# Optimization experiments

Measured on AMD Instinct MI355X. Metric: run time of the kernel, lower is better.

The kernel has to match this reference:

```python
import jax, jax.numpy as jnp
import numpy as np

V, D, H, L, S, B, FF, MAXLEN = 50257, 768, 12, 12, 1024, 4, 3072, 1024
HD = D // H
EPS = 1e-5


def layernorm(x, w, b):
    m = jnp.mean(x, axis=-1, keepdims=True)
    v = jnp.mean(jnp.square(x - m), axis=-1, keepdims=True)
    return (x - m) * jax.lax.rsqrt(v + EPS) * w + b


def setup_inputs() -> dict:
    key = jax.random.key(0)
    ks = jax.random.split(key, 8)
    std = 0.02
    return {
        "tokens": jax.random.randint(ks[0], (B, S), 0, V, dtype=jnp.int32),
        "wte": std * jax.random.normal(ks[1], (V, D), jnp.float32),
        "wpe": std * jax.random.normal(ks[2], (1, MAXLEN, D), jnp.float32),
        "ln1_w": jnp.ones((L, D), jnp.float32),
        "ln1_b": jnp.zeros((L, D), jnp.float32),
        "ln2_w": jnp.ones((L, D), jnp.float32),
        "ln2_b": jnp.zeros((L, D), jnp.float32),
        "W_exp": std * jax.random.normal(ks[3], (L, D, 3 * D), jnp.float32),
        "b_exp": jnp.zeros((L, 3 * D), jnp.float32),
        "W_o": std * jax.random.normal(ks[4], (L, D, D), jnp.float32),
        "b_o": jnp.zeros((L, D), jnp.float32),
        "W_ff1": std * jax.random.normal(ks[5], (L, D, FF), jnp.float32),
        "b_ff1": jnp.zeros((L, FF), jnp.float32),
        "W_ff2": std * jax.random.normal(ks[6], (L, FF, D), jnp.float32),
        "b_ff2": jnp.zeros((L, D), jnp.float32),
    }


def reference(tokens, wte, wpe, ln1_w, ln1_b, ln2_w, ln2_b,
              W_exp, b_exp, W_o, b_o, W_ff1, b_ff1, W_ff2, b_ff2):
    Bc, Sc = tokens.shape
    x = wte[tokens] + wpe[:, :Sc, :]                      # [B,S,D]
    mask = jnp.tril(jnp.ones((Sc, Sc), bool))             # causal (past=None)
    scale = 1.0 / jnp.sqrt(jnp.float32(HD))
    presents = []
    for l in range(L):
        h = layernorm(x, ln1_w[l], ln1_b[l])
        qkv = h @ W_exp[l] + b_exp[l]                     # [B,S,3D]
        q, k, v = jnp.split(qkv, 3, axis=-1)
        q = q.reshape(Bc, Sc, H, HD)
        k = k.reshape(Bc, Sc, H, HD)
        v = v.reshape(Bc, Sc, H, HD)
        presents.append(jnp.stack([k, v]))                # [2,B,S,H,HD]
        score = jnp.einsum('bqhd,bkhd->bhqk', q, k)
        score = jnp.where(mask, score, jnp.float32(-1e20))
        attn = jax.nn.softmax(score * scale, axis=-1)     # mask applied BEFORE scaling, as in source
        a = jnp.einsum('bhqk,bkhd->bqhd', attn, v).reshape(Bc, Sc, D)
        a = a @ W_o[l] + b_o[l]
        add = layernorm(a + x, ln2_w[l], ln2_b[l])        # LN2 on residual sum (GPT2-variant in source)
        ff = jax.nn.gelu(add @ W_ff1[l] + b_ff1[l], approximate=False)
        ff = ff @ W_ff2[l] + b_ff2[l]
        x = ff + add
    return x, jnp.stack(presents)                         # [L,2,B,S,H,HD]
```

## Files before the change

### kernel.cpp

```cpp
#include <hip/hip_runtime.h>
#include <hip/hip_bf16.h>
#include <math.h>

#define Bc 4
#define Sc 1024
#define Dc 768
#define Hc 12
#define Lc 12
#define FFc 3072
#define Mtot (Bc*Sc)

typedef __bf16 bf16x8 __attribute__((ext_vector_type(8)));
typedef __bf16 bf16x4 __attribute__((ext_vector_type(4)));
typedef float f32x4 __attribute__((ext_vector_type(4)));

__device__ __forceinline__ void gload_lds16(const void* g, void* l) {
    __builtin_amdgcn_global_load_lds((const __attribute__((address_space(1))) void*)g,
                                     (__attribute__((address_space(3))) void*)l, 16, 0, 0);
}

template <int N>
__device__ __forceinline__ void waitcnt_vm() {
    if constexpr (N == 0)       asm volatile("s_waitcnt vmcnt(0)" ::: "memory");
    else if constexpr (N == 4)  asm volatile("s_waitcnt vmcnt(4)" ::: "memory");
    else if constexpr (N == 5)  asm volatile("s_waitcnt vmcnt(5)" ::: "memory");
    else if constexpr (N == 8)  asm volatile("s_waitcnt vmcnt(8)" ::: "memory");
    else if constexpr (N == 10) asm volatile("s_waitcnt vmcnt(10)" ::: "memory");
    else static_assert(N == 0, "unsupported vmcnt");
}

__global__ __launch_bounds__(256) void embed_kernel(const int* __restrict__ tokens,
                                                    const float* __restrict__ wte,
                                                    const float* __restrict__ wpe,
                                                    float* __restrict__ x) {
    int row = blockIdx.x;
    int s = row & (Sc - 1);
    int tok = tokens[row];
    const float* wt = wte + (size_t)tok * Dc;
    const float* wp = wpe + (size_t)s * Dc;
    float* xr = x + (size_t)row * Dc;
#pragma unroll
    for (int k = 0; k < 3; ++k) {
        int d = threadIdx.x + k * 256;
        xr[d] = wt[d] + wp[d];
    }
}

__global__ __launch_bounds__(256) void prep_kernel(
        const float* __restrict__ We, const float* __restrict__ Wo,
        const float* __restrict__ Wf1, const float* __restrict__ Wf2,
        __bf16* __restrict__ Te, __bf16* __restrict__ To,
        __bf16* __restrict__ Tf1, __bf16* __restrict__ Tf2,
        const float* __restrict__ x, const float* __restrict__ lw,
        const float* __restrict__ lb, __bf16* __restrict__ outb) {
    __shared__ float shm[64 * 69];
    int bid = blockIdx.x;
    int t = threadIdx.x;
    if (bid < 1728) {
        const float* W; __bf16* T; int K, N, tt;
        if (bid < 432)       { W = We;  T = Te;  K = 768;  N = 2304; tt = bid; }
        else if (bid < 576)  { W = Wo;  T = To;  K = 768;  N = 768;  tt = bid - 432; }
        else if (bid < 1152) { W = Wf1; T = Tf1; K = 768;  N = 3072; tt = bid - 576; }
        else                 { W = Wf2; T = Tf2; K = 3072; N = 768;  tt = bid - 1152; }
        int nx = N >> 6;
        int n0 = (tt % nx) * 64, k0 = (tt / nx) * 64;
        int cx = (t & 15) * 4, ry = t >> 4;
#pragma unroll
        for (int i = 0; i < 4; ++i) {
            int r = ry + 16 * i;
            float4 v = *(const float4*)(W + (size_t)(k0 + r) * N + n0 + cx);
            shm[r * 69 + cx + 0] = v.x; shm[r * 69 + cx + 1] = v.y;
            shm[r * 69 + cx + 2] = v.z; shm[r * 69 + cx + 3] = v.w;
        }
        __syncthreads();
        int kc = (t & 15) * 4, ny = t >> 4;
#pragma unroll
        for (int i = 0; i < 4; ++i) {
            int nr = ny + 16 * i;
            bf16x4 o;
#pragma unroll
            for (int j = 0; j < 4; ++j)
                o[j] = (__bf16)shm[(kc + j) * 69 + nr];
            *(bf16x4*)(T + (size_t)(n0 + nr) * K + k0 + kc) = o;
        }
    } else {
        int row = bid - 1728;
        size_t ro = (size_t)row * Dc;
        float4 v;
        float s1 = 0.0f, s2 = 0.0f;
        if (t < 192) {
            v = *(const float4*)(x + ro + t * 4);
            s1 = v.x + v.y + v.z + v.w;
            s2 = v.x * v.x + v.y * v.y + v.z * v.z + v.w * v.w;
#pragma unroll
            for (int o = 32; o; o >>= 1) {
                s1 += __shfl_down(s1, o);
                s2 += __shfl_down(s2, o);
            }
            if ((t & 63) == 0) { shm[t >> 6] = s1; shm[3 + (t >> 6)] = s2; }
        }
        __syncthreads();
        if (t < 192) {
            float S1 = shm[0] + shm[1] + shm[2];
            float S2 = shm[3] + shm[4] + shm[5];
            float mean = S1 * (1.0f / Dc);
            float var = S2 * (1.0f / Dc) - mean * mean;
            float rs = rsqrtf(var + 1e-5f);
            const float4 w4 = *(const float4*)(lw + t * 4);
            const float4 b4 = *(const float4*)(lb + t * 4);
            bf16x4 o;
            o[0] = (__bf16)((v.x - mean) * rs * w4.x + b4.x);
            o[1] = (__bf16)((v.y - mean) * rs * w4.y + b4.y);
            o[2] = (__bf16)((v.z - mean) * rs * w4.z + b4.z);
            o[3] = (__bf16)((v.w - mean) * rs * w4.w + b4.w);
            *(bf16x4*)(outb + ro + t * 4) = o;
        }
    }
}

__global__ __launch_bounds__(192) void ln2_kernel(const float* __restrict__ x,
                                                  const float* __restrict__ lw,
                                                  const float* __restrict__ lb,
                                                  __bf16* __restrict__ outb,
                                                  float* __restrict__ outf) {
    __shared__ float red[6];
    int row = blockIdx.x;
    size_t ro = (size_t)row * Dc;
    int t = threadIdx.x;
    float4 v = *(const float4*)(x + ro + t * 4);
    float s1 = v.x + v.y + v.z + v.w;
    float s2 = v.x * v.x + v.y * v.y + v.z * v.z + v.w * v.w;
#pragma unroll
    for (int o = 32; o; o >>= 1) {
        s1 += __shfl_down(s1, o);
        s2 += __shfl_down(s2, o);
    }
    if ((t & 63) == 0) { red[t >> 6] = s1; red[3 + (t >> 6)] = s2; }
    __syncthreads();
    float S1 = red[0] + red[1] + red[2];
    float S2 = red[3] + red[4] + red[5];
    float mean = S1 * (1.0f / Dc);
    float var = S2 * (1.0f / Dc) - mean * mean;
    float rs = rsqrtf(var + 1e-5f);
    const float4 w4 = *(const float4*)(lw + t * 4);
    const float4 b4 = *(const float4*)(lb + t * 4);
    float o0 = (v.x - mean) * rs * w4.x + b4.x;
    float o1 = (v.y - mean) * rs * w4.y + b4.y;
    float o2 = (v.z - mean) * rs * w4.z + b4.z;
    float o3 = (v.w - mean) * rs * w4.w + b4.w;
    bf16x4 ob; ob[0] = (__bf16)o0; ob[1] = (__bf16)o1; ob[2] = (__bf16)o2; ob[3] = (__bf16)o3;
    *(bf16x4*)(outb + ro + t * 4) = ob;
    *(float4*)(outf + ro + t * 4) = make_float4(o0, o1, o2, o3);
}

template <int BMr, int BNc, int BK, int EPI>
__global__ __launch_bounds__(256) void gemm_bf16(const __bf16* __restrict__ A,
                                                 const __bf16* __restrict__ BT,
                                                 const float* __restrict__ bias,
                                                 const float* __restrict__ addin,
                                                 float* __restrict__ Cf,
                                                 __bf16* __restrict__ Cb,
                                                 float* __restrict__ pres,
                                                 int K, int N) {
    constexpr int HRm = BMr / 32, HRn = BNc / 32;
    constexpr int KS  = BK / 32;
    constexpr int LPR = BK / 8;
    constexpr int SSH = (BK == 32) ? 1 : 0;
    constexpr int IA  = BMr * BK / 2048;
    constexpr int IB  = BNc * BK / 2048;
    constexpr int S1w = IA + IB;
    static_assert(IA * 2048 == BMr * BK && IB * 2048 == BNc * BK, "staging granularity");
    __shared__ __bf16 As[3][BMr * BK];
    __shared__ __bf16 Bs[3][BNc * BK];
    int tid = threadIdx.x;
    int w = tid >> 6, l = tid & 63;
    int wrow = (w >> 1) * (BMr / 2), wcol = (w & 1) * (BNc / 2);
    int brow0 = blockIdx.x * BMr, bcol0 = blockIdx.y * BNc;
    int rsel = l & 15, lg = l >> 4;

    f32x4 acc[HRm][HRn] = {};

    const __bf16* Abase = A + (size_t)brow0 * K;
    const __bf16* Bbase = BT + (size_t)bcol0 * K;

    auto stage = [&](int buf, int kt) {
#pragma unroll
        for (int i = 0; i < IA; ++i) {
            int cid = i * 256 + tid;
            int row = cid / LPR, slot = cid % LPR;
            int chunk = slot ^ ((row >> SSH) & (LPR - 1));
            gload_lds16(Abase + (size_t)row * K + kt + chunk * 8,
                        &As[buf][(i * 256 + w * 64) * 8]);
        }
#pragma unroll
        for (int i = 0; i < IB; ++i) {
            int cid = i * 256 + tid;
            int row = cid / LPR, slot = cid % LPR;
            int chunk = slot ^ ((row >> SSH) & (LPR - 1));
            gload_lds16(Bbase + (size_t)row * K + kt + chunk * 8,
                        &Bs[buf][(i * 256 + w * 64) * 8]);
        }
    };

    int nk = K / BK;
    stage(0, 0);
    stage(1, BK);
    int cur = 0;
    for (int kt = 0; kt < nk; ++kt) {
        if (kt + 2 < nk) {
            int b2 = cur + 2; if (b2 >= 3) b2 -= 3;
            stage(b2, (kt + 2) * BK);
            waitcnt_vm<2 * S1w>();
        } else if (kt + 1 < nk) {
            waitcnt_vm<S1w>();
        } else {
            waitcnt_vm<0>();
        }
        __builtin_amdgcn_s_barrier();
        __builtin_amdgcn_sched_barrier(0);

        bf16x8 af[KS][HRm], bfr[KS][HRn];
#pragma unroll
        for (int m = 0; m < HRm; ++m) {
            int r = wrow + m * 16 + rsel;
            int sw = (r >> SSH) & (LPR - 1);
#pragma unroll
            for (int s = 0; s < KS; ++s)
                af[s][m] = *(const bf16x8*)(&As[cur][r * BK + ((s * 4 + lg) ^ sw) * 8]);
        }
#pragma unroll
        for (int n = 0; n < HRn; ++n) {
            int r = wcol + n * 16 + rsel;
            int sw = (r >> SSH) & (LPR - 1);
#pragma unroll
            for (int s = 0; s < KS; ++s)
                bfr[s][n] = *(const bf16x8*)(&Bs[cur][r * BK + ((s * 4 + lg) ^ sw) * 8]);
        }
#pragma unroll
        for (int s = 0; s < KS; ++s)
#pragma unroll
            for (int m = 0; m < HRm; ++m)
#pragma unroll
                for (int n = 0; n < HRn; ++n)
                    acc[m][n] = __builtin_amdgcn_mfma_f32_16x16x32_bf16(af[s][m], bfr[s][n], acc[m][n], 0, 0, 0);

        __builtin_amdgcn_sched_barrier(0);
        __builtin_amdgcn_s_barrier();
        cur = (cur == 2) ? 0 : cur + 1;
    }

    int r4 = lg * 4, cc = rsel;
#pragma unroll
    for (int m = 0; m < HRm; ++m)
#pragma unroll
        for (int n = 0; n < HRn; ++n) {
            int col = bcol0 + wcol + n * 16 + cc;
            float bv = bias[col];
#pragma unroll
            for (int i = 0; i < 4; ++i) {
                int row = brow0 + wrow + m * 16 + r4 + i;
                float v = acc[m][n][i] + bv;
                if (EPI == 1) {
                    v += addin[(size_t)row * N + col];
                    Cf[(size_t)row * N + col] = v;
                }
                if (EPI == 2) {
                    float u = 0.7978845608f * (v + 0.044715f * v * v * v);
                    v = v / (1.0f + __expf(-2.0f * u));
                    Cb[(size_t)row * N + col] = (__bf16)v;
                }
                if (EPI == 3) {
                    Cb[(size_t)row * N + col] = (__bf16)v;
                    if (col >= 768) {
                        int kv = (col >= 1536) ? 1 : 0;
                        pres[((size_t)kv * Mtot + row) * Dc + (col - 768 - kv * 768)] = v;
                    }
                }
            }
        }
}

__global__ __launch_bounds__(256) void attn_mfma_kernel(const __bf16* __restrict__ qkvb,
                                                        __bf16* __restrict__ aout) {
    __shared__ __bf16 Ks[64 * 72];
    __shared__ __bf16 Vts[64 * 72];
    __shared__ __bf16 Ps[4][16 * 72];
    int bh = blockIdx.x;
    int b = bh / Hc, h = bh % Hc;
    int qt = (Sc / 64 - 1) - blockIdx.y;
    int tid = threadIdx.x;
    int w = tid >> 6, l = tid & 63;
    int lr = l & 15, lg = l >> 4;
    int qb = qt * 64;

    const __bf16* base = qkvb + (size_t)b * Sc * 2304 + h * 64;

    bf16x8 qf[2];
    {
        const __bf16* qrow = base + (size_t)(qb + w * 16 + lr) * 2304 + lg * 8;
        qf[0] = *(const bf16x8*)(qrow);
        qf[1] = *(const bf16x8*)(qrow + 32);
    }

    f32x4 O[4] = {};
    float mrow[4], lrowv[4];
#pragma unroll
    for (int i = 0; i < 4; ++i) { mrow[i] = -1e30f; lrowv[i] = 0.0f; }

    int kj = tid >> 2, kc = tid & 3;
    int vj = tid & 63, vd0 = (tid >> 6) * 8;

    for (int t = 0; t <= qt; ++t) {
        __syncthreads();
#pragma unroll
        for (int it = 0; it < 2; ++it) {
            int c = kc + 4 * it;
            bf16x8 v = *(const bf16x8*)(base + (size_t)(t * 64 + kj) * 2304 + 768 + c * 8);
            *(bf16x8*)(&Ks[kj * 72 + c * 8]) = v;
        }
#pragma unroll
        for (int it = 0; it < 2; ++it) {
            int d0 = vd0 + 32 * it;
            bf16x8 v = *(const bf16x8*)(base + (size_t)(t * 64 + vj) * 2304 + 1536 + d0);
#pragma unroll
            for (int i = 0; i < 8; ++i)
                Vts[(d0 + i) * 72 + vj] = v[i];
        }
        __syncthreads();

        f32x4 sc[4] = {};
        __builtin_amdgcn_s_setprio(1);
#pragma unroll
        for (int s = 0; s < 2; ++s)
#pragma unroll
            for (int n = 0; n < 4; ++n) {
                bf16x8 kf = *(const bf16x8*)(&Ks[(n * 16 + lr) * 72 + s * 32 + lg * 8]);
                sc[n] = __builtin_amdgcn_mfma_f32_16x16x32_bf16(qf[s], kf, sc[n], 0, 0, 0);
            }
        __builtin_amdgcn_s_setprio(0);

        bool diag = (t == qt);
#pragma unroll
        for (int n = 0; n < 4; ++n)
#pragma unroll
            for (int i = 0; i < 4; ++i) {
                float s = sc[n][i] * 0.125f;
                if (diag) {
                    int jg = n * 16 + lr;
                    int qg = w * 16 + lg * 4 + i;
                    if (jg > qg) s = -1e30f;
                }
                sc[n][i] = s;
            }
        float corr[4], psum[4];
#pragma unroll
        for (int i = 0; i < 4; ++i) {
            float mx = fmaxf(fmaxf(sc[0][i], sc[1][i]), fmaxf(sc[2][i], sc[3][i]));
#pragma unroll
            for (int o = 1; o < 16; o <<= 1) mx = fmaxf(mx, __shfl_xor(mx, o));
            float mnew = fmaxf(mrow[i], mx);
            corr[i] = __expf(mrow[i] - mnew);
            mrow[i] = mnew;
            psum[i] = 0.0f;
        }
#pragma unroll
        for (int n = 0; n < 4; ++n)
#pragma unroll
            for (int i = 0; i < 4; ++i) {
                float p = __expf(sc[n][i] - mrow[i]);
                psum[i] += p;
                Ps[w][(lg * 4 + i) * 72 + n * 16 + lr] = (__bf16)p;
            }
#pragma unroll
        for (int i = 0; i < 4; ++i) {
#pragma unroll
            for (int o = 1; o < 16; o <<= 1) psum[i] += __shfl_xor(psum[i], o);
            lrowv[i] = lrowv[i] * corr[i] + psum[i];
        }
#pragma unroll
        for (int n = 0; n < 4; ++n)
#pragma unroll
            for (int i = 0; i < 4; ++i) O[n][i] *= corr[i];
        __builtin_amdgcn_s_setprio(1);
#pragma unroll
        for (int s = 0; s < 2; ++s) {
            bf16x8 pf = *(const bf16x8*)(&Ps[w][lr * 72 + s * 32 + lg * 8]);
#pragma unroll
            for (int n = 0; n < 4; ++n) {
                bf16x8 vf = *(const bf16x8*)(&Vts[(n * 16 + lr) * 72 + s * 32 + lg * 8]);
                O[n] = __builtin_amdgcn_mfma_f32_16x16x32_bf16(pf, vf, O[n], 0, 0, 0);
            }
        }
        __builtin_amdgcn_s_setprio(0);
    }
    __bf16* orow = aout + (size_t)(b * Sc + qb + w * 16 + lg * 4) * Dc + h * 64 + lr;
#pragma unroll
    for (int n = 0; n < 4; ++n)
#pragma unroll
        for (int i = 0; i < 4; ++i)
            orow[(size_t)i * Dc + n * 16] = (__bf16)(O[n][i] / lrowv[i]);
}

extern "C" void kernel_launch(void* const* d_in, const int* in_sizes, int n_in,
                              void* d_out, int out_size, void* d_ws, size_t ws_size,
                              hipStream_t stream) {
    const int*   tokens = (const int*)d_in[0];
    const float* wte    = (const float*)d_in[1];
    const float* wpe    = (const float*)d_in[2];
    const float* ln1_w  = (const float*)d_in[3];
    const float* ln1_b  = (const float*)d_in[4];
    const float* ln2_w  = (const float*)d_in[5];
    const float* ln2_b  = (const float*)d_in[6];
    const float* W_exp  = (const float*)d_in[7];
    const float* b_exp  = (const float*)d_in[8];
    const float* W_o    = (const float*)d_in[9];
    const float* b_o    = (const float*)d_in[10];
    const float* W_ff1  = (const float*)d_in[11];
    const float* b_ff1  = (const float*)d_in[12];
    const float* W_ff2  = (const float*)d_in[13];
    const float* b_ff2  = (const float*)d_in[14];

    float* out_x    = (float*)d_out;
    float* out_pres = out_x + (size_t)Mtot * Dc;

    float* ws   = (float*)d_ws;
    float* x    = ws;
    float* addf = x + (size_t)Mtot * Dc;
    __bf16* hb   = (__bf16*)(addf + (size_t)Mtot * Dc);
    __bf16* addb = hb + (size_t)Mtot * Dc;
    __bf16* qkvb = addb + (size_t)Mtot * Dc;
    __bf16* ff1b = qkvb + (size_t)Mtot * 3 * Dc;
    __bf16* wt_exp = ff1b + (size_t)Mtot * FFc;
    __bf16* wt_o   = wt_exp + (size_t)2304 * 768;
    __bf16* wt_ff1 = wt_o   + (size_t)768 * 768;
    __bf16* wt_ff2 = wt_ff1 + (size_t)3072 * 768;

    embed_kernel<<<Mtot, 256, 0, stream>>>(tokens, wte, wpe, x);

    for (int lidx = 0; lidx < Lc; ++lidx) {
        prep_kernel<<<1728 + Mtot, 256, 0, stream>>>(
            W_exp + (size_t)lidx * 768 * 2304, W_o + (size_t)lidx * 768 * 768,
            W_ff1 + (size_t)lidx * 768 * 3072, W_ff2 + (size_t)lidx * 3072 * 768,
            wt_exp, wt_o, wt_ff1, wt_ff2,
            x, ln1_w + lidx * Dc, ln1_b + lidx * Dc, hb);

        gemm_bf16<64, 192, 32, 3><<<dim3(Mtot / 64, 2304 / 192), 256, 0, stream>>>(
            hb, wt_exp, b_exp + (size_t)lidx * 3 * Dc,
            nullptr, nullptr, qkvb, out_pres + (size_t)lidx * 2 * Mtot * Dc, 768, 2304);
        attn_mfma_kernel<<<dim3(Bc * Hc, Sc / 64), 256, 0, stream>>>(qkvb, hb);
        gemm_bf16<64, 96, 64, 1><<<dim3(Mtot / 64, 768 / 96), 256, 0, stream>>>(
            hb, wt_o, b_o + (size_t)lidx * Dc,
            x, x, nullptr, nullptr, 768, 768);
        ln2_kernel<<<Mtot, 192, 0, stream>>>(
            x, ln2_w + lidx * Dc, ln2_b + lidx * Dc, addb, addf);
        gemm_bf16<128, 128, 32, 2><<<dim3(Mtot / 128, FFc / 128), 256, 0, stream>>>(
            addb, wt_ff1, b_ff1 + (size_t)lidx * FFc,
            nullptr, nullptr, ff1b, nullptr, 768, FFc);
        float* ff2dst = (lidx == Lc - 1) ? out_x : x;
        gemm_bf16<64, 96, 64, 1><<<dim3(Mtot / 64, 768 / 96), 256, 0, stream>>>(
            ff1b, wt_ff2, b_ff2 + (size_t)lidx * Dc,
            addf, ff2dst, nullptr, nullptr, 3072, 768);
    }
}
```

Measured before the change: 2.020 ms.

## Widen attention blocks to 128 queries with 8 waves sharing K/V tiles

The attention kernel now runs 512 threads per block covering 128 query rows, so each K/V tile loaded into LDS is reused by twice as many waves. Grid y halves, and the two half-blocks skip tiles past their causal diagonal while still joining the shared loads. The V transpose store changes to paired 2-element writes instead of scalar writes. This halves global K/V traffic per query, at the cost of idle waves in the upper half-block on its last tile and fewer blocks in flight.

Result: slower. 2.112 ms (+4.6%).

```diff
diff --git a/kernel.cpp b/kernel.cpp
--- a/kernel.cpp
+++ b/kernel.cpp
@@ -12,6 +12,7 @@
 
 typedef __bf16 bf16x8 __attribute__((ext_vector_type(8)));
 typedef __bf16 bf16x4 __attribute__((ext_vector_type(4)));
+typedef __bf16 bf16x2 __attribute__((ext_vector_type(2)));
 typedef float f32x4 __attribute__((ext_vector_type(4)));
 
 __device__ __forceinline__ void gload_lds16(const void* g, void* l) {
@@ -280,18 +281,20 @@
         }
 }
 
-__global__ __launch_bounds__(256) void attn_mfma_kernel(const __bf16* __restrict__ qkvb,
+__global__ __launch_bounds__(512) void attn_mfma_kernel(const __bf16* __restrict__ qkvb,
                                                         __bf16* __restrict__ aout) {
     __shared__ __bf16 Ks[64 * 72];
     __shared__ __bf16 Vts[64 * 72];
-    __shared__ __bf16 Ps[4][16 * 72];
+    __shared__ __bf16 Ps[8][16 * 72];
     int bh = blockIdx.x;
     int b = bh / Hc, h = bh % Hc;
-    int qt = (Sc / 64 - 1) - blockIdx.y;
+    int qt = (Sc / 128 - 1) - blockIdx.y;
     int tid = threadIdx.x;
     int w = tid >> 6, l = tid & 63;
     int lr = l & 15, lg = l >> 4;
-    int qb = qt * 64;
+    int qb = qt * 128;
+    int hh = w >> 2;
+    int qgb = (w & 3) * 16 + lg * 4;
 
     const __bf16* base = qkvb + (size_t)b * Sc * 2304 + h * 64;
 
@@ -307,26 +310,28 @@
 #pragma unroll
     for (int i = 0; i < 4; ++i) { mrow[i] = -1e30f; lrowv[i] = 0.0f; }
 
-    int kj = tid >> 2, kc = tid & 3;
-    int vj = tid & 63, vd0 = (tid >> 6) * 8;
-
-    for (int t = 0; t <= qt; ++t) {
+    int kj = tid >> 3, kc = tid & 7;
+    int vj0 = (tid & 31) * 2, vd0 = (tid >> 5) * 4;
+
+    int ntiles = 2 * qt + 2;
+    for (int t = 0; t < ntiles; ++t) {
         __syncthreads();
-#pragma unroll
-        for (int it = 0; it < 2; ++it) {
-            int c = kc + 4 * it;
-            bf16x8 v = *(const bf16x8*)(base + (size_t)(t * 64 + kj) * 2304 + 768 + c * 8);
-            *(bf16x8*)(&Ks[kj * 72 + c * 8]) = v;
-        }
-#pragma unroll
-        for (int it = 0; it < 2; ++it) {
-            int d0 = vd0 + 32 * it;
-            bf16x8 v = *(const bf16x8*)(base + (size_t)(t * 64 + vj) * 2304 + 1536 + d0);
-#pragma unroll
-            for (int i = 0; i < 8; ++i)
-                Vts[(d0 + i) * 72 + vj] = v[i];
+        {
+            bf16x8 v = *(const bf16x8*)(base + (size_t)(t * 64 + kj) * 2304 + 768 + kc * 8);
+            *(bf16x8*)(&Ks[kj * 72 + kc * 8]) = v;
+        }
+        {
+            bf16x4 a0 = *(const bf16x4*)(base + (size_t)(t * 64 + vj0) * 2304 + 1536 + vd0);
+            bf16x4 a1 = *(const bf16x4*)(base + (size_t)(t * 64 + vj0 + 1) * 2304 + 1536 + vd0);
+#pragma unroll
+            for (int i = 0; i < 4; ++i) {
+                bf16x2 o; o[0] = a0[i]; o[1] = a1[i];
+                *(bf16x2*)(&Vts[(vd0 + i) * 72 + vj0]) = o;
+            }
         }
         __syncthreads();
+
+        if (t > 2 * qt + hh) continue;
 
         f32x4 sc[4] = {};
         __builtin_amdgcn_s_setprio(1);
@@ -339,7 +344,7 @@
             }
         __builtin_amdgcn_s_setprio(0);
 
-        bool diag = (t == qt);
+        bool diag = (t == 2 * qt + hh);
 #pragma unroll
         for (int n = 0; n < 4; ++n)
 #pragma unroll
@@ -347,8 +352,7 @@
                 float s = sc[n][i] * 0.125f;
                 if (diag) {
                     int jg = n * 16 + lr;
-                    int qg = w * 16 + lg * 4 + i;
-                    if (jg > qg) s = -1e30f;
+                    if (jg > qgb + i) s = -1e30f;
                 }
                 sc[n][i] = s;
             }
@@ -447,7 +451,7 @@
         gemm_bf16<64, 192, 32, 3><<<dim3(Mtot / 64, 2304 / 192), 256, 0, stream>>>(
             hb, wt_exp, b_exp + (size_t)lidx * 3 * Dc,
             nullptr, nullptr, qkvb, out_pres + (size_t)lidx * 2 * Mtot * Dc, 768, 2304);
-        attn_mfma_kernel<<<dim3(Bc * Hc, Sc / 64), 256, 0, stream>>>(qkvb, hb);
+        attn_mfma_kernel<<<dim3(Bc * Hc, Sc / 128), 512, 0, stream>>>(qkvb, hb);
         gemm_bf16<64, 96, 64, 1><<<dim3(Mtot / 64, 768 / 96), 256, 0, stream>>>(
             hb, wt_o, b_o + (size_t)lidx * Dc,
             x, x, nullptr, nullptr, 768, 768);
```
